# Performance work log

Hardware: AMD Instinct MI355X
Metric: run time of the kernel (lower is better)

Reference implementation:

```python
import jax, jax.numpy as jnp
import numpy as np

N_NODES = 100000


def _gcn_layer(h_in, W, b, src, dst, norm, num_nodes):
    # PyG GCNConv: linear transform first, then normalized scatter-add aggregation
    h = h_in @ W                                   # [N, out_dim]
    msg = h[src] * norm[:, None]                   # gather + scale over edges
    out = jax.ops.segment_sum(msg, dst, num_segments=num_nodes)
    return out + b


def setup_inputs() -> dict:
    key = jax.random.key(0)
    k1, k2, k3, k4, k5 = jax.random.split(key, 5)
    d_in, d_hid, d_out = 128, 128, 128
    x = jax.random.normal(k1, (N_NODES, d_in), dtype=jnp.float32)
    edge_index = jax.random.randint(k2, (2, 1600000), 0, N_NODES, dtype=jnp.int64)
    # Glorot-ish init for weights, zeros for bias (as in GCNConv defaults)
    W1 = jax.random.normal(k3, (d_in, d_hid), dtype=jnp.float32) / np.sqrt(d_in)
    b1 = jnp.zeros((d_hid,), dtype=jnp.float32)
    W2 = jax.random.normal(k4, (d_hid, d_out), dtype=jnp.float32) / np.sqrt(d_hid)
    b2 = jnp.zeros((d_out,), dtype=jnp.float32)
    return {"x": x, "edge_index": edge_index, "W1": W1, "b1": b1, "W2": W2, "b2": b2}


def reference(x, edge_index, W1, b1, W2, b2):
    num_nodes = x.shape[0]
    # Add self-loops (GCNConv default add_self_loops=True)
    loop = jnp.arange(num_nodes, dtype=edge_index.dtype)
    src = jnp.concatenate([edge_index[0], loop])
    dst = jnp.concatenate([edge_index[1], loop])
    # Symmetric normalization: deg^{-1/2}[src] * deg^{-1/2}[dst]
    deg = jax.ops.segment_sum(jnp.ones_like(dst, dtype=x.dtype), dst, num_segments=num_nodes)
    dinv = jnp.where(deg > 0, jax.lax.rsqrt(deg), 0.0)
    norm = dinv[src] * dinv[dst]                   # [E + N]

    h = _gcn_layer(x, W1, b1, src, dst, norm, num_nodes)
    h = jax.nn.relu(h)                             # dropout is identity in eval mode
    out = _gcn_layer(h, W2, b2, src, dst, norm, num_nodes)
    return out
```

## Files before the change

kernel.cpp:

```cpp
#include <hip/hip_runtime.h>


#define DIM 128
#define CAP 192
typedef unsigned short ushort_t;
typedef unsigned int uint_t;
typedef __attribute__((ext_vector_type(8))) short bf16x8;
typedef __attribute__((ext_vector_type(4))) float f32x4;

static __device__ __forceinline__ uint_t f2bf(float f) {
    union { float f; uint_t u; } c; c.f = f;
    uint_t u = c.u;
    return (u + 0x7FFFu + ((u >> 16) & 1u)) >> 16;
}
static __device__ __forceinline__ float bf2f(uint_t h) {
    union { uint_t u; float f; } c; c.u = h << 16;
    return c.f;
}
static __device__ __forceinline__ float as_f(uint_t u) {
    union { uint_t u; float f; } c; c.u = u;
    return c.f;
}
static __device__ __forceinline__ void gld16(const void* g, void* l) {
    __builtin_amdgcn_global_load_lds(
        (const __attribute__((address_space(1))) uint_t*)g,
        (__attribute__((address_space(3))) uint_t*)l, 16, 0, 0);
}

__global__ __launch_bounds__(256) void k_bin(const int* __restrict__ src,
                                             const int* __restrict__ dst,
                                             int* __restrict__ bcur,
                                             uint_t* __restrict__ stage,
                                             int E, int RB) {
    int e = blockIdx.x * 256 + threadIdx.x;
    if (e >= E) return;
    int slice = blockIdx.x & 31;
    int s = src[e], d = dst[e];
    int idx = slice * RB + (d >> 7);
    int c = atomicAdd(&bcur[idx], 1);
    if (c < CAP)
        stage[(size_t)idx * CAP + c] = (uint_t)((s << 7) | (d & 127));
}

__global__ __launch_bounds__(1024) void k_bscan(const int* __restrict__ bcur,
                                                int* __restrict__ bbase, int RB) {
    __shared__ int sdat[1024];
    int t = threadIdx.x;
    int v = 0;
    if (t < RB)
        #pragma unroll
        for (int s = 0; s < 32; ++s) v += min(bcur[s * RB + t], CAP);
    sdat[t] = v;
    __syncthreads();
    #pragma unroll
    for (int o = 1; o < 1024; o <<= 1) {
        int x = (t >= o) ? sdat[t - o] : 0;
        __syncthreads();
        sdat[t] += x;
        __syncthreads();
    }
    if (t < RB) bbase[t] = sdat[t] - v;
}

__global__ __launch_bounds__(256) void k_build(const uint_t* __restrict__ stage,
                                               const int* __restrict__ bcur,
                                               const int* __restrict__ bbase,
                                               int* __restrict__ off,
                                               float* __restrict__ dinv,
                                               int* __restrict__ csr_src,
                                               int RB, int N, int E) {
    __shared__ int scnt[33];
    __shared__ int cnt[128], excl[128], lcur[128];
    __shared__ uint_t ent[32 * CAP];
    int b = blockIdx.x, t = threadIdx.x;
    if (t < 32) scnt[t + 1] = min(bcur[t * RB + b], CAP);
    if (t == 0) scnt[0] = 0;
    if (t < 128) { cnt[t] = 0; lcur[t] = 0; }
    __syncthreads();
    if (t == 0)
        for (int s = 1; s <= 32; ++s) scnt[s] += scnt[s - 1];
    __syncthreads();
    int total = scnt[32];
    for (int s = 0; s < 32; ++s) {
        int c0 = scnt[s], c1 = scnt[s + 1];
        const uint_t* sp = stage + (size_t)(s * RB + b) * CAP - c0;
        for (int i = c0 + t; i < c1; i += 256) ent[i] = sp[i];
    }
    __syncthreads();
    for (int i = t; i < total; i += 256) atomicAdd(&cnt[ent[i] & 127], 1);
    __syncthreads();
    if (t < 128) excl[t] = cnt[t];
    __syncthreads();
    #pragma unroll
    for (int o = 1; o < 128; o <<= 1) {
        int x = 0;
        if (t < 128 && t >= o) x = excl[t - o];
        __syncthreads();
        if (t < 128) excl[t] += x;
        __syncthreads();
    }
    int base = bbase[b];
    if (t < 128) {
        excl[t] -= cnt[t];
        int node = (b << 7) + t;
        if (node < N) {
            off[node] = base + excl[t];
            dinv[node] = rsqrtf((float)cnt[t] + 1.0f);
        }
    }
    if (b == RB - 1 && t == 0) off[N] = E;
    __syncthreads();
    for (int i = t; i < total; i += 256) {
        uint_t v = ent[i];
        int dl = v & 127;
        int pos = base + excl[dl] + atomicAdd(&lcur[dl], 1);
        csr_src[pos] = (int)(v >> 7);
    }
}

__global__ __launch_bounds__(256) void k_prep(const float* __restrict__ W1,
                                              const float* __restrict__ W2,
                                              const float* __restrict__ x,
                                              short* __restrict__ whi,
                                              short* __restrict__ wlo,
                                              short* __restrict__ xhi,
                                              short* __restrict__ xlo,
                                              int N, int nxc) {
    int t = threadIdx.x;
    if (blockIdx.x < 16) {
        int g = blockIdx.x * 256 + t;
        int layer = g >> 11, c = g & 2047;
        const float* W = layer ? W2 : W1;
        int ks = c >> 9, nt = (c >> 6) & 7, l = c & 63;
        int q = l >> 4, m = l & 15;
        int n = nt * 16 + m;
        bf16x8 h8, l8;
        #pragma unroll
        for (int j = 0; j < 8; ++j) {
            int k = ks * 32 + q * 8 + j;
            float f = W[k * 128 + n];
            uint_t hb = f2bf(f);
            h8[j] = (short)hb;
            l8[j] = (short)f2bf(f - bf2f(hb));
        }
        ((bf16x8*)whi)[g] = h8;
        ((bf16x8*)wlo)[g] = l8;
    } else {
        int c = (blockIdx.x - 16) * 256 + t;
        if (c >= nxc) return;
        int lane = c & 63, p = (c >> 6) & 7, kslab = (c >> 9) & 3, rb = c >> 11;
        int row = rb * 128 + p * 16 + (lane & 15);
        int k0 = kslab * 32 + (lane >> 4) * 8;
        bf16x8 h8 = {}, l8 = {};
        if (row < N) {
            float4 fa = ((const float4*)x)[row * 32 + (k0 >> 2)];
            float4 fb = ((const float4*)x)[row * 32 + (k0 >> 2) + 1];
            float f[8] = {fa.x, fa.y, fa.z, fa.w, fb.x, fb.y, fb.z, fb.w};
            #pragma unroll
            for (int j = 0; j < 8; ++j) {
                uint_t hb = f2bf(f[j]);
                h8[j] = (short)hb;
                l8[j] = (short)f2bf(f[j] - bf2f(hb));
            }
        }
        ((bf16x8*)xhi)[c] = h8;
        ((bf16x8*)xlo)[c] = l8;
    }
}

__global__ __launch_bounds__(256) void k_gemm(const short* __restrict__ afhi,
                                              const short* __restrict__ aflo,
                                              const short* __restrict__ wfhi,
                                              const short* __restrict__ wflo,
                                              ushort_t* __restrict__ hout, int M) {
    __shared__ short AH[8192], AL[8192], WH[8192], WL[8192];
    const int t = threadIdx.x;
    const int rb = blockIdx.x;
    const int wv = t >> 6, l = t & 63;
    const int mb = (wv & 1) * 4;
    const int nbc = (wv >> 1) * 4;

    f32x4 acc[4][4];
    #pragma unroll
    for (int i = 0; i < 4; ++i)
        #pragma unroll
        for (int j = 0; j < 4; ++j)
            acc[i][j] = (f32x4){0.f, 0.f, 0.f, 0.f};

    #pragma unroll
    for (int kc = 0; kc < 2; ++kc) {
        if (kc) __syncthreads();
        {
            const short* ga = afhi + (size_t)(rb * 4 + 2 * kc) * 4096;
            const short* gb = aflo + (size_t)(rb * 4 + 2 * kc) * 4096;
            const short* gh = wfhi + 2 * kc * 4096;
            const short* gl = wflo + 2 * kc * 4096;
            #pragma unroll
            for (int i = 0; i < 4; ++i) {
                int idx = (i * 256 + t) * 8;
                gld16(ga + idx, AH + idx);
                gld16(gb + idx, AL + idx);
                gld16(gh + idx, WH + idx);
                gld16(gl + idx, WL + idx);
            }
        }
        __syncthreads();
        #pragma unroll
        for (int ksl = 0; ksl < 2; ++ksl) {
            bf16x8 ah[4], al[4];
            #pragma unroll
            for (int i = 0; i < 4; ++i) {
                ah[i] = *(const bf16x8*)&AH[((ksl * 8 + mb + i) * 64 + l) * 8];
                al[i] = *(const bf16x8*)&AL[((ksl * 8 + mb + i) * 64 + l) * 8];
            }
            #pragma unroll
            for (int j = 0; j < 4; ++j) {
                bf16x8 bh = *(const bf16x8*)&WH[((ksl * 8 + nbc + j) * 64 + l) * 8];
                bf16x8 bl = *(const bf16x8*)&WL[((ksl * 8 + nbc + j) * 64 + l) * 8];
                #pragma unroll
                for (int i = 0; i < 4; ++i) {
                    acc[i][j] = __builtin_amdgcn_mfma_f32_16x16x32_bf16(ah[i], bh, acc[i][j], 0, 0, 0);
                    acc[i][j] = __builtin_amdgcn_mfma_f32_16x16x32_bf16(al[i], bh, acc[i][j], 0, 0, 0);
                    acc[i][j] = __builtin_amdgcn_mfma_f32_16x16x32_bf16(ah[i], bl, acc[i][j], 0, 0, 0);
                }
            }
        }
    }

    const int q = l >> 4, mm = l & 15;
    #pragma unroll
    for (int i = 0; i < 4; ++i)
        #pragma unroll
        for (int r = 0; r < 4; ++r) {
            int gr = rb * 128 + (wv & 1) * 64 + i * 16 + q * 4 + r;
            if (gr < M) {
                #pragma unroll
                for (int j = 0; j < 4; ++j)
                    hout[gr * 128 + nbc * 16 + j * 16 + mm] =
                        (ushort_t)f2bf(acc[i][j][r]);
            }
        }
}

template <int FRAG>
__global__ __launch_bounds__(256) void k_agg(const uint_t* __restrict__ h32,
                                             const int* __restrict__ off,
                                             const int* __restrict__ csr_src,
                                             const float* __restrict__ dinv,
                                             const float* __restrict__ bias,
                                             float* __restrict__ out,
                                             uint_t* __restrict__ fhi,
                                             uint_t* __restrict__ flo, int N) {
    int n = (blockIdx.x * 256 + threadIdx.x) >> 6;
    if (n >= N) return;
    int l = threadIdx.x & 63;

    float di = dinv[n];
    uint_t sv = h32[(n << 6) + l];
    float accx = as_f(sv << 16) * di;
    float accy = as_f(sv & 0xffff0000u) * di;

    int e = off[n], end = off[n + 1];
    for (; e + 8 <= end; e += 8) {
        int s[8]; float ws[8]; uint_t v[8];
        #pragma unroll
        for (int u = 0; u < 8; ++u) s[u] = csr_src[e + u];
        #pragma unroll
        for (int u = 0; u < 8; ++u) { ws[u] = dinv[s[u]]; v[u] = h32[(s[u] << 6) + l]; }
        #pragma unroll
        for (int u = 0; u < 8; ++u) {
            accx += ws[u] * as_f(v[u] << 16);
            accy += ws[u] * as_f(v[u] & 0xffff0000u);
        }
    }
    for (; e < end; ++e) {
        int s = csr_src[e];
        float w = dinv[s];
        uint_t v = h32[(s << 6) + l];
        accx += w * as_f(v << 16);
        accy += w * as_f(v & 0xffff0000u);
    }

    float2 bv = ((const float2*)bias)[l];
    accx = di * accx + bv.x;
    accy = di * accy + bv.y;

    if (FRAG) {
        accx = fmaxf(accx, 0.f);
        accy = fmaxf(accy, 0.f);
        uint_t hx = f2bf(accx), hy = f2bf(accy);
        uint_t lx = f2bf(accx - bf2f(hx)), ly = f2bf(accy - bf2f(hy));
        int rb = n >> 7, kslab = l >> 4, p = (n >> 4) & 7;
        int lp = ((l >> 2) & 3) * 16 + (n & 15);
        int chunk = ((rb * 4 + kslab) * 8 + p) * 64 + lp;
        fhi[chunk * 4 + (l & 3)] = (hy << 16) | hx;
        flo[chunk * 4 + (l & 3)] = (ly << 16) | lx;
    } else {
        ((float2*)out)[(n << 6) + l] = make_float2(accx, accy);
    }
}

extern "C" void kernel_launch(void* const* d_in, const int* in_sizes, int n_in,
                              void* d_out, int out_size, void* d_ws, size_t ws_size,
                              hipStream_t stream) {
    const float* x  = (const float*)d_in[0];
    const int*   ei = (const int*)d_in[1];
    const float* W1 = (const float*)d_in[2];
    const float* b1 = (const float*)d_in[3];
    const float* W2 = (const float*)d_in[4];
    const float* b2 = (const float*)d_in[5];
    float* out = (float*)d_out;

    const int N = in_sizes[0] / DIM;
    const int E = in_sizes[1] / 2;
    const int* src = ei;
    const int* dst = ei + E;
    const int RB = (N + 127) / 128;
    const int nxc = RB * 2048;

    char* w = (char*)d_ws;
    float* dinv    = (float*)(w);
    int*   bcur    = (int*)  (w + (1 << 19));
    int*   bbase   = (int*)  (w + (1 << 19) + (1 << 17));
    int*   off     = (int*)  (w + (3 << 19));
    short* whi     = (short*)(w + (1 << 21) + (1 << 13));
    short* wlo     = whi + 2 * 16384;
    int*   csr_src = (int*)  (w + ((size_t)5 << 19));
    short* fhi     = (short*)(w + ((size_t)17 << 20));
    short* flo     = (short*)(w + ((size_t)43 << 20));
    ushort_t* hbuf = (ushort_t*)(w + ((size_t)69 << 20));
    uint_t* stage  = (uint_t*)hbuf;

    const int B = 256;
    const int agg_grid = (N * 64 + B - 1) / B;

    hipMemsetAsync(bcur, 0, (size_t)32 * RB * 4, stream);
    k_prep<<<16 + (nxc + B - 1) / B, B, 0, stream>>>(W1, W2, x, whi, wlo,
                                                     fhi, flo, N, nxc);
    k_bin<<<(E + B - 1) / B, B, 0, stream>>>(src, dst, bcur, stage, E, RB);
    k_bscan<<<1, 1024, 0, stream>>>(bcur, bbase, RB);
    k_build<<<RB, B, 0, stream>>>(stage, bcur, bbase, off, dinv, csr_src,
                                  RB, N, E);
    k_gemm<<<RB, B, 0, stream>>>(fhi, flo, whi, wlo, hbuf, N);
    k_agg<1><<<agg_grid, B, 0, stream>>>((const uint_t*)hbuf, off, csr_src,
                                         dinv, b1, nullptr,
                                         (uint_t*)fhi, (uint_t*)flo, N);
    k_gemm<<<RB, B, 0, stream>>>(fhi, flo, whi + 16384, wlo + 16384, hbuf, N);
    k_agg<0><<<agg_grid, B, 0, stream>>>((const uint_t*)hbuf, off, csr_src,
                                         dinv, b2, out,
                                         nullptr, nullptr, N);
}
```

Measured before the change: 398.9 us.

## Fold source-degree scaling into GEMM epilogue and switch A operand to swizzled row layout

The GEMM epilogue now multiplies each output row by dinv before the bf16 store. This removes the per-edge dinv[src] gather and multiply from the aggregation loop, which is also unrolled to 16 edges. The A-operand fragment layout changes to a row-major layout with an XOR swizzle across 16-byte chunks, produced by both the prep and aggregation kernels, and the GEMM's LDS reads follow the new swizzle. Nontemporal loads and stores are added on streaming paths. Rounding to bf16 now happens after the dinv scaling, which slightly changes numerics.

```diff
diff --git a/kernel.cpp b/kernel.cpp
--- a/kernel.cpp
+++ b/kernel.cpp
@@ -7,6 +7,7 @@
 typedef unsigned int uint_t;
 typedef __attribute__((ext_vector_type(8))) short bf16x8;
 typedef __attribute__((ext_vector_type(4))) float f32x4;
+typedef __attribute__((ext_vector_type(2))) float f32x2;
 
 static __device__ __forceinline__ uint_t f2bf(float f) {
     union { float f; uint_t u; } c; c.f = f;
@@ -148,14 +149,13 @@
     } else {
         int c = (blockIdx.x - 16) * 256 + t;
         if (c >= nxc) return;
-        int lane = c & 63, p = (c >> 6) & 7, kslab = (c >> 9) & 3, rb = c >> 11;
-        int row = rb * 128 + p * 16 + (lane & 15);
-        int k0 = kslab * 32 + (lane >> 4) * 8;
+        int rb = c >> 11, row = (c >> 4) & 127, cc = c & 15;
+        int node = rb * 128 + row;
         bf16x8 h8 = {}, l8 = {};
-        if (row < N) {
-            float4 fa = ((const float4*)x)[row * 32 + (k0 >> 2)];
-            float4 fb = ((const float4*)x)[row * 32 + (k0 >> 2) + 1];
-            float f[8] = {fa.x, fa.y, fa.z, fa.w, fb.x, fb.y, fb.z, fb.w};
+        if (node < N) {
+            f32x4 fa = __builtin_nontemporal_load((const f32x4*)x + node * 32 + cc * 2);
+            f32x4 fb = __builtin_nontemporal_load((const f32x4*)x + node * 32 + cc * 2 + 1);
+            float f[8] = {fa[0], fa[1], fa[2], fa[3], fb[0], fb[1], fb[2], fb[3]};
             #pragma unroll
             for (int j = 0; j < 8; ++j) {
                 uint_t hb = f2bf(f[j]);
@@ -163,8 +163,10 @@
                 l8[j] = (short)f2bf(f[j] - bf2f(hb));
             }
         }
-        ((bf16x8*)xhi)[c] = h8;
-        ((bf16x8*)xlo)[c] = l8;
+        int pos = (cc & 8) | ((cc & 7) ^ (row & 7));
+        int slot = rb * 2048 + row * 16 + pos;
+        __builtin_nontemporal_store(h8, (bf16x8*)xhi + slot);
+        __builtin_nontemporal_store(l8, (bf16x8*)xlo + slot);
     }
 }
 
@@ -172,6 +174,7 @@
                                               const short* __restrict__ aflo,
                                               const short* __restrict__ wfhi,
                                               const short* __restrict__ wflo,
+                                              const float* __restrict__ dinv,
                                               ushort_t* __restrict__ hout, int M) {
     __shared__ short AH[8192], AL[8192], WH[8192], WL[8192];
     const int t = threadIdx.x;
@@ -191,17 +194,18 @@
     for (int kc = 0; kc < 2; ++kc) {
         if (kc) __syncthreads();
         {
-            const short* ga = afhi + (size_t)(rb * 4 + 2 * kc) * 4096;
-            const short* gb = aflo + (size_t)(rb * 4 + 2 * kc) * 4096;
+            const short* ga = afhi + (size_t)rb * 16384;
+            const short* gb = aflo + (size_t)rb * 16384;
             const short* gh = wfhi + 2 * kc * 4096;
             const short* gl = wflo + 2 * kc * 4096;
             #pragma unroll
             for (int i = 0; i < 4; ++i) {
-                int idx = (i * 256 + t) * 8;
-                gld16(ga + idx, AH + idx);
-                gld16(gb + idx, AL + idx);
-                gld16(gh + idx, WH + idx);
-                gld16(gl + idx, WL + idx);
+                int idx = i * 256 + t;
+                int goff = ((idx >> 3) * 16 + kc * 8 + (idx & 7)) * 8;
+                gld16(ga + goff, AH + idx * 8);
+                gld16(gb + goff, AL + idx * 8);
+                gld16(gh + idx * 8, WH + idx * 8);
+                gld16(gl + idx * 8, WL + idx * 8);
             }
         }
         __syncthreads();
@@ -210,8 +214,11 @@
             bf16x8 ah[4], al[4];
             #pragma unroll
             for (int i = 0; i < 4; ++i) {
-                ah[i] = *(const bf16x8*)&AH[((ksl * 8 + mb + i) * 64 + l) * 8];
-                al[i] = *(const bf16x8*)&AL[((ksl * 8 + mb + i) * 64 + l) * 8];
+                int rowl = (mb + i) * 16 + (l & 15);
+                int cA = ksl * 4 + (l >> 4);
+                int sa = rowl * 64 + ((cA ^ (rowl & 7)) << 3);
+                ah[i] = *(const bf16x8*)&AH[sa];
+                al[i] = *(const bf16x8*)&AL[sa];
             }
             #pragma unroll
             for (int j = 0; j < 4; ++j) {
@@ -234,10 +241,11 @@
         for (int r = 0; r < 4; ++r) {
             int gr = rb * 128 + (wv & 1) * 64 + i * 16 + q * 4 + r;
             if (gr < M) {
+                float di = dinv[gr];
                 #pragma unroll
                 for (int j = 0; j < 4; ++j)
                     hout[gr * 128 + nbc * 16 + j * 16 + mm] =
-                        (ushort_t)f2bf(acc[i][j][r]);
+                        (ushort_t)f2bf(di * acc[i][j][r]);
             }
         }
 }
@@ -254,34 +262,46 @@
     int n = (blockIdx.x * 256 + threadIdx.x) >> 6;
     if (n >= N) return;
     int l = threadIdx.x & 63;
+    const uint_t* hl = h32 + l;
 
     float di = dinv[n];
-    uint_t sv = h32[(n << 6) + l];
-    float accx = as_f(sv << 16) * di;
-    float accy = as_f(sv & 0xffff0000u) * di;
+    f32x2 bv = *((const f32x2*)bias + l);
+    uint_t sv = hl[(size_t)n << 6];
+    float accx = as_f(sv << 16);
+    float accy = as_f(sv & 0xffff0000u);
 
     int e = off[n], end = off[n + 1];
-    for (; e + 8 <= end; e += 8) {
-        int s[8]; float ws[8]; uint_t v[8];
-        #pragma unroll
-        for (int u = 0; u < 8; ++u) s[u] = csr_src[e + u];
-        #pragma unroll
-        for (int u = 0; u < 8; ++u) { ws[u] = dinv[s[u]]; v[u] = h32[(s[u] << 6) + l]; }
+    for (; e + 16 <= end; e += 16) {
+        int s[16]; uint_t v[16];
+        #pragma unroll
+        for (int u = 0; u < 16; ++u) s[u] = __builtin_nontemporal_load(&csr_src[e + u]);
+        #pragma unroll
+        for (int u = 0; u < 16; ++u) v[u] = hl[(size_t)s[u] << 6];
+        #pragma unroll
+        for (int u = 0; u < 16; ++u) {
+            accx += as_f(v[u] << 16);
+            accy += as_f(v[u] & 0xffff0000u);
+        }
+    }
+    if (e + 8 <= end) {
+        int s[8]; uint_t v[8];
+        #pragma unroll
+        for (int u = 0; u < 8; ++u) s[u] = __builtin_nontemporal_load(&csr_src[e + u]);
+        #pragma unroll
+        for (int u = 0; u < 8; ++u) v[u] = hl[(size_t)s[u] << 6];
         #pragma unroll
         for (int u = 0; u < 8; ++u) {
-            accx += ws[u] * as_f(v[u] << 16);
-            accy += ws[u] * as_f(v[u] & 0xffff0000u);
-        }
+            accx += as_f(v[u] << 16);
+            accy += as_f(v[u] & 0xffff0000u);
+        }
+        e += 8;
     }
     for (; e < end; ++e) {
-        int s = csr_src[e];
-        float w = dinv[s];
-        uint_t v = h32[(s << 6) + l];
-        accx += w * as_f(v << 16);
-        accy += w * as_f(v & 0xffff0000u);
-    }
-
-    float2 bv = ((const float2*)bias)[l];
+        uint_t v = hl[(size_t)csr_src[e] << 6];
+        accx += as_f(v << 16);
+        accy += as_f(v & 0xffff0000u);
+    }
+
     accx = di * accx + bv.x;
     accy = di * accy + bv.y;
 
@@ -290,13 +310,14 @@
         accy = fmaxf(accy, 0.f);
         uint_t hx = f2bf(accx), hy = f2bf(accy);
         uint_t lx = f2bf(accx - bf2f(hx)), ly = f2bf(accy - bf2f(hy));
-        int rb = n >> 7, kslab = l >> 4, p = (n >> 4) & 7;
-        int lp = ((l >> 2) & 3) * 16 + (n & 15);
-        int chunk = ((rb * 4 + kslab) * 8 + p) * 64 + lp;
-        fhi[chunk * 4 + (l & 3)] = (hy << 16) | hx;
-        flo[chunk * 4 + (l & 3)] = (ly << 16) | lx;
+        int rb = n >> 7, row = n & 127, cc = l >> 2;
+        int pos = (cc & 8) | ((cc & 7) ^ (row & 7));
+        size_t iu = ((size_t)rb << 13) + row * 64 + pos * 4 + (l & 3);
+        __builtin_nontemporal_store((hy << 16) | hx, &fhi[iu]);
+        __builtin_nontemporal_store((ly << 16) | lx, &flo[iu]);
     } else {
-        ((float2*)out)[(n << 6) + l] = make_float2(accx, accy);
+        f32x2 o; o.x = accx; o.y = accy;
+        __builtin_nontemporal_store(o, (f32x2*)out + ((size_t)n << 6) + l);
     }
 }
 
@@ -341,11 +362,11 @@
     k_bscan<<<1, 1024, 0, stream>>>(bcur, bbase, RB);
     k_build<<<RB, B, 0, stream>>>(stage, bcur, bbase, off, dinv, csr_src,
                                   RB, N, E);
-    k_gemm<<<RB, B, 0, stream>>>(fhi, flo, whi, wlo, hbuf, N);
+    k_gemm<<<RB, B, 0, stream>>>(fhi, flo, whi, wlo, dinv, hbuf, N);
     k_agg<1><<<agg_grid, B, 0, stream>>>((const uint_t*)hbuf, off, csr_src,
                                          dinv, b1, nullptr,
                                          (uint_t*)fhi, (uint_t*)flo, N);
-    k_gemm<<<RB, B, 0, stream>>>(fhi, flo, whi + 16384, wlo + 16384, hbuf, N);
+    k_gemm<<<RB, B, 0, stream>>>(fhi, flo, whi + 16384, wlo + 16384, dinv, hbuf, N);
     k_agg<0><<<agg_grid, B, 0, stream>>>((const uint_t*)hbuf, off, csr_src,
                                          dinv, b2, out,
                                          nullptr, nullptr, N);
```

Result: slower. 408.4 us (+2.4%).
